# Optimization experiments

Measured on AMD Instinct MI355X. Metric: run time of the kernel, lower is better.

Reference implementation:

```python
import jax, jax.numpy as jnp
from jax import lax
import numpy as np

C_IN, C_OUT, K, STRIDE = 256, 512, 3, 1
EPS = 1e-5


def setup_inputs() -> dict:
    key = jax.random.key(0)
    ks = jax.random.split(key, 8)
    B, H, W = 32, 56, 56
    x = jax.random.normal(ks[0], (B, C_IN, H, W), dtype=jnp.float32)
    dw_w = jax.random.normal(ks[1], (C_IN, 1, K, K), dtype=jnp.float32) * 0.1
    dw_b = jax.random.normal(ks[2], (C_IN,), dtype=jnp.float32) * 0.05
    g1 = jnp.ones((C_IN,), dtype=jnp.float32)
    b1 = jnp.zeros((C_IN,), dtype=jnp.float32)
    pw_w = jax.random.normal(ks[3], (C_OUT, C_IN), dtype=jnp.float32) * (1.0 / np.sqrt(C_IN))
    pw_b = jax.random.normal(ks[4], (C_OUT,), dtype=jnp.float32) * 0.05
    g2 = jnp.ones((C_OUT,), dtype=jnp.float32)
    b2 = jnp.zeros((C_OUT,), dtype=jnp.float32)
    return {"x": x, "dw_w": dw_w, "dw_b": dw_b, "g1": g1, "b1": b1,
            "pw_w": pw_w, "pw_b": pw_b, "g2": g2, "b2": b2}


def _batchnorm(x, gamma, beta):
    # training-mode BN over (N, H, W) per channel, matching fresh nn.BatchNorm2d
    mean = jnp.mean(x, axis=(0, 2, 3), keepdims=True)
    var = jnp.var(x, axis=(0, 2, 3), keepdims=True)
    xn = (x - mean) * lax.rsqrt(var + EPS)
    return xn * gamma[None, :, None, None] + beta[None, :, None, None]


def reference(x, dw_w, dw_b, g1, b1, pw_w, pw_b, g2, b2):
    p = K // 2
    # reflect padding (padding_mode='reflect' in torch Conv2d)
    xp = jnp.pad(x, ((0, 0), (0, 0), (p, p), (p, p)), mode='reflect')
    # grouped depthwise conv: one filter per channel
    y = lax.conv_general_dilated(
        xp, dw_w, window_strides=(STRIDE, STRIDE), padding='VALID',
        dimension_numbers=('NCHW', 'OIHW', 'NCHW'),
        feature_group_count=C_IN)
    y = y + dw_b[None, :, None, None]
    y = jax.nn.relu(_batchnorm(y, g1, b1))
    # pointwise 1x1 conv == channel GEMM
    z = jnp.einsum('bchw,oc->bohw', y, pw_w) + pw_b[None, :, None, None]
    z = jax.nn.relu(_batchnorm(z, g2, b2))
    return z
```

## Files before the change

kernel.cpp:

```cpp
#include <hip/hip_runtime.h>
#include <hip/hip_bf16.h>
#include <stdint.h>


#define CIN   256
#define COUT  512
#define BATCH 32
#define HH    56
#define WWID  56
#define HWSZ  3136
#define NTOT  100352
#define NHWF  100352.0f
#define EPSV  1e-5f

typedef __bf16 bf16;
typedef __bf16 bf16x8 __attribute__((ext_vector_type(8)));
typedef float  f32x4  __attribute__((ext_vector_type(4)));

#define WS_STATS1   0
#define WS_SCALE1   2048
#define WS_SHIFT1   3072
#define WS_YSUM     4096
#define WS_S2       5120
#define WS_T2       7168
#define WS_G        16384
#define WS_WBF      278528
#define WS_YT       540672

__device__ __forceinline__ void gload16(const void* g, void* l) {
  __builtin_amdgcn_global_load_lds((const __attribute__((address_space(1))) void*)g,
                                   (__attribute__((address_space(3))) void*)l, 16, 0, 0);
}

__global__ __launch_bounds__(256) void k1_dwstats(const float* __restrict__ x,
                                                  const float* __restrict__ dww,
                                                  float* __restrict__ stats1) {
  __shared__ float plane[HWSZ];
  __shared__ float red[8];
  int bid = blockIdx.x;
  int c = bid & (CIN - 1);
  int b = bid >> 8;
  const float4* xp4 = (const float4*)(x + ((size_t)(b * CIN + c)) * HWSZ);
  float4* pl4 = (float4*)plane;
  for (int i = threadIdx.x; i < HWSZ / 4; i += 256) pl4[i] = xp4[i];
  float w9[9];
#pragma unroll
  for (int q = 0; q < 9; ++q) w9[q] = dww[c * 9 + q];
  __syncthreads();
  float s = 0.f, sq = 0.f;
  for (int p = threadIdx.x; p < HWSZ; p += 256) {
    int h = p / WWID;
    int w = p - h * WWID;
    float acc = 0.f;
#pragma unroll
    for (int dy = 0; dy < 3; ++dy) {
      int hh = h - 1 + dy;
      hh = hh < 0 ? 1 : (hh > 55 ? 54 : hh);
#pragma unroll
      for (int dx = 0; dx < 3; ++dx) {
        int ww2 = w - 1 + dx;
        ww2 = ww2 < 0 ? 1 : (ww2 > 55 ? 54 : ww2);
        acc += w9[dy * 3 + dx] * plane[hh * WWID + ww2];
      }
    }
    s += acc; sq += acc * acc;
  }
#pragma unroll
  for (int m = 1; m < 64; m <<= 1) { s += __shfl_xor(s, m); sq += __shfl_xor(sq, m); }
  int wv = threadIdx.x >> 6;
  if ((threadIdx.x & 63) == 0) { red[wv] = s; red[4 + wv] = sq; }
  __syncthreads();
  if (threadIdx.x == 0) {
    atomicAdd(&stats1[c],        red[0] + red[1] + red[2] + red[3]);
    atomicAdd(&stats1[CIN + c],  red[4] + red[5] + red[6] + red[7]);
  }
}

__global__ __launch_bounds__(256) void k2_finalize1(const float* __restrict__ stats1,
                                                    const float* __restrict__ g1,
                                                    const float* __restrict__ b1,
                                                    const float* __restrict__ pww,
                                                    float* __restrict__ scale1,
                                                    float* __restrict__ shift1,
                                                    bf16* __restrict__ wbf) {
  int blk = blockIdx.x, t = threadIdx.x;
  if (blk == 0) {
    float mean = stats1[t] * (1.0f / NHWF);
    float var  = stats1[CIN + t] * (1.0f / NHWF) - mean * mean;
    float sc = g1[t] * rsqrtf(var + EPSV);
    scale1[t] = sc;
    shift1[t] = b1[t] - mean * sc;
  } else {
    int o = blk - 1;
    wbf[o * CIN + t] = (bf16)pww[o * CIN + t];
  }
}

__global__ __launch_bounds__(256) void k3_normT(const float* __restrict__ x,
                                                const float* __restrict__ dww,
                                                const float* __restrict__ scale1,
                                                const float* __restrict__ shift1,
                                                bf16* __restrict__ yt) {
  __shared__ float xt[64][3][58];
  __shared__ __align__(16) bf16 outt[56][64];
  int bid = blockIdx.x;
  int cg = bid & 3;
  int h  = (bid >> 2) % 56;
  int b  = bid / 224;
  int c0 = cg * 64;
  int hr0 = (h == 0) ? 1 : h - 1;
  int hr2 = (h == 55) ? 54 : h + 1;
  for (int idx = threadIdx.x; idx < 64 * 3 * 56; idx += 256) {
    int c = idx / 168;
    int rem = idx - c * 168;
    int r = rem / 56;
    int w = rem - r * 56;
    int hr = (r == 0) ? hr0 : ((r == 1) ? h : hr2);
    xt[c][r][w + 1] = x[((size_t)((b * CIN + c0 + c) * HH + hr)) * WWID + w];
  }
  __syncthreads();
  if (threadIdx.x < 192) {
    int c = threadIdx.x / 3, r = threadIdx.x % 3;
    xt[c][r][0]  = xt[c][r][2];
    xt[c][r][57] = xt[c][r][55];
  }
  __syncthreads();
  int c  = threadIdx.x >> 2;
  int wq = threadIdx.x & 3;
  float w9[9];
#pragma unroll
  for (int q = 0; q < 9; ++q) w9[q] = dww[(c0 + c) * 9 + q];
  float sc = scale1[c0 + c], sh = shift1[c0 + c];
  for (int w = wq; w < 56; w += 4) {
    float acc = 0.f;
#pragma unroll
    for (int r = 0; r < 3; ++r) {
      const float* row = &xt[c][r][w];
      acc += w9[r * 3 + 0] * row[0] + w9[r * 3 + 1] * row[1] + w9[r * 3 + 2] * row[2];
    }
    float v = fmaxf(acc * sc + sh, 0.f);
    outt[w][c] = (bf16)v;
  }
  __syncthreads();
  for (int idx = threadIdx.x; idx < 56 * 8; idx += 256) {
    int w = idx >> 3, part = idx & 7;
    uint4 v = *(const uint4*)(&outt[w][part * 8]);
    *(uint4*)(yt + ((size_t)(b * HWSZ + h * WWID + w)) * CIN + c0 + part * 8) = v;
  }
}

__global__ __launch_bounds__(256) void kg_gram(const bf16* __restrict__ yt,
                                               float* __restrict__ G,
                                               float* __restrict__ ysum) {
  __shared__ __align__(16) unsigned short yTl[256 * 64];
  int bid = blockIdx.x;
  int job = bid & 3;
  int chunk = bid >> 2;
  int qa = job >> 1, qb = job & 1;
  int tid = threadIdx.x;
  int wv = tid >> 6, l = tid & 63;
  int wm = wv >> 1, wn = wv & 1;
  f32x4 acc[4][4];
#pragma unroll
  for (int mi = 0; mi < 4; ++mi)
#pragma unroll
    for (int ni = 0; ni < 4; ++ni) acc[mi][ni] = (f32x4){0.f, 0.f, 0.f, 0.f};
  float ys = 0.f;
  int r_loc = tid >> 2;
  int ci0 = tid & 3;
  int rs_k[8];
#pragma unroll
  for (int k = 0; k < 8; ++k) rs_k[k] = (r_loc & 7) | (((r_loc >> 3) ^ k) << 3);

  for (int it = 0; it < 16; ++it) {
    const unsigned short* src = (const unsigned short*)yt + ((size_t)chunk * 1024 + it * 64 + r_loc) * CIN;
#pragma unroll
    for (int u = 0; u < 8; ++u) {
      int c0 = (ci0 + u * 4) * 8;
      unsigned short v8[8];
      *(uint4*)v8 = *(const uint4*)(src + c0);
#pragma unroll
      for (int k = 0; k < 8; ++k) yTl[(c0 + k) * 64 + rs_k[k]] = v8[k];
    }
    __syncthreads();
#pragma unroll
    for (int kk = 0; kk < 2; ++kk) {
      bf16x8 af[4], bfr[4];
      int rc = kk * 4 + (l >> 4);
#pragma unroll
      for (int mi = 0; mi < 4; ++mi) {
        int c = qa * 128 + wm * 64 + mi * 16 + (l & 15);
        af[mi] = *(const bf16x8*)(yTl + c * 64 + ((rc ^ (c & 7)) << 3));
      }
#pragma unroll
      for (int ni = 0; ni < 4; ++ni) {
        int c = qb * 128 + wn * 64 + ni * 16 + (l & 15);
        bfr[ni] = *(const bf16x8*)(yTl + c * 64 + ((rc ^ (c & 7)) << 3));
      }
#pragma unroll
      for (int mi = 0; mi < 4; ++mi)
#pragma unroll
        for (int ni = 0; ni < 4; ++ni)
          acc[mi][ni] = __builtin_amdgcn_mfma_f32_16x16x32_bf16(af[mi], bfr[ni], acc[mi][ni], 0, 0, 0);
    }
    if (job == 0) {
      const bf16* row = (const bf16*)(yTl + tid * 64);
#pragma unroll
      for (int i = 0; i < 64; ++i) ys += (float)row[i];
    }
    __syncthreads();
  }
#pragma unroll
  for (int mi = 0; mi < 4; ++mi)
#pragma unroll
    for (int ni = 0; ni < 4; ++ni)
#pragma unroll
      for (int j = 0; j < 4; ++j) {
        int m = qa * 128 + wm * 64 + mi * 16 + (l >> 4) * 4 + j;
        int n = qb * 128 + wn * 64 + ni * 16 + (l & 15);
        atomicAdd(&G[m * 256 + n], acc[mi][ni][j]);
      }
  if (job == 0) atomicAdd(&ysum[tid], ys);
}

__global__ __launch_bounds__(256) void k2c_fin2(const float* __restrict__ G,
                                                const float* __restrict__ ysum,
                                                const bf16* __restrict__ wbf,
                                                const float* __restrict__ g2,
                                                const float* __restrict__ b2,
                                                float* __restrict__ s2,
                                                float* __restrict__ t2) {
  __shared__ float wl[256];
  __shared__ float red[8];
  int o = blockIdx.x, t = threadIdx.x;
  wl[t] = (float)wbf[o * 256 + t];
  __syncthreads();
  float gw = 0.f;
  for (int c = 0; c < 256; ++c) gw += G[c * 256 + t] * wl[c];
  float msq_p  = gw * wl[t];
  float mean_p = wl[t] * ysum[t];
#pragma unroll
  for (int m = 1; m < 64; m <<= 1) { msq_p += __shfl_xor(msq_p, m); mean_p += __shfl_xor(mean_p, m); }
  int wv = t >> 6;
  if ((t & 63) == 0) { red[wv] = msq_p; red[4 + wv] = mean_p; }
  __syncthreads();
  if (t == 0) {
    float msq  = (red[0] + red[1] + red[2] + red[3]) * (1.0f / NHWF);
    float mean = (red[4] + red[5] + red[6] + red[7]) * (1.0f / NHWF);
    float var  = msq - mean * mean;
    float sc = g2[o] * rsqrtf(var + EPSV);
    s2[o] = sc;
    t2[o] = b2[o] - mean * sc;
  }
}

__global__ __launch_bounds__(256) void k4_gemm(const bf16* __restrict__ wbf,
                                               const bf16* __restrict__ yt,
                                               const float* __restrict__ s2,
                                               const float* __restrict__ t2,
                                               float* __restrict__ out) {
  __shared__ __align__(16) unsigned char LDSBUF[32768];
  __shared__ float s2l[128], t2l[128];
  unsigned char* Als = LDSBUF;
  unsigned char* Bls = LDSBUF + 16384;
  int wg = blockIdx.x;
  int newid = (wg & 7) * 392 + (wg >> 3);
  int mt    = newid & 3;
  int ntile = newid >> 2;
  int tid = threadIdx.x;
  int wv = tid >> 6, l = tid & 63;
  int wm = wv >> 1, wn = wv & 1;
  if (tid < 128) { s2l[tid] = s2[mt * 128 + tid]; t2l[tid] = t2[mt * 128 + tid]; }
  f32x4 acc[4][4];
#pragma unroll
  for (int mi = 0; mi < 4; ++mi)
#pragma unroll
    for (int ni = 0; ni < 4; ++ni) acc[mi][ni] = (f32x4){0.f, 0.f, 0.f, 0.f};
  const char* wb = (const char*)wbf;
  const char* yb = (const char*)yt + (size_t)ntile * 128 * CIN * 2;

  for (int k0 = 0; k0 < 256; k0 += 64) {
#pragma unroll
    for (int i = 0; i < 4; ++i) {
      int q = i * 256 + wv * 64 + l;
      int row = q >> 3, pp = q & 7;
      int cc = pp ^ (row & 7);
      gload16(wb + ((size_t)(mt * 128 + row) * CIN + k0) * 2 + cc * 16,
              Als + i * 4096 + wv * 1024);
      gload16(yb + ((size_t)row * CIN + k0) * 2 + cc * 16,
              Bls + i * 4096 + wv * 1024);
    }
    __syncthreads();
#pragma unroll
    for (int kk = 0; kk < 2; ++kk) {
      bf16x8 af[4], bfr[4];
#pragma unroll
      for (int mi = 0; mi < 4; ++mi) {
        int row = wm * 64 + mi * 16 + (l & 15);
        int ck = kk * 4 + (l >> 4);
        af[mi] = *(const bf16x8*)(Als + row * 128 + ((ck ^ (row & 7)) << 4));
      }
#pragma unroll
      for (int ni = 0; ni < 4; ++ni) {
        int row = wn * 64 + ni * 16 + (l & 15);
        int ck = kk * 4 + (l >> 4);
        bfr[ni] = *(const bf16x8*)(Bls + row * 128 + ((ck ^ (row & 7)) << 4));
      }
#pragma unroll
      for (int mi = 0; mi < 4; ++mi)
#pragma unroll
        for (int ni = 0; ni < 4; ++ni)
          acc[mi][ni] = __builtin_amdgcn_mfma_f32_16x16x32_bf16(af[mi], bfr[ni], acc[mi][ni], 0, 0, 0);
    }
    __syncthreads();
  }

#pragma unroll
  for (int mi = 0; mi < 4; ++mi)
#pragma unroll
    for (int ni = 0; ni < 4; ++ni)
#pragma unroll
      for (int j = 0; j < 4; ++j) {
        int ol = wm * 64 + mi * 16 + (l >> 4) * 4 + j;
        int r_flat = ntile * 128 + wn * 64 + ni * 16 + (l & 15);
        int b  = r_flat / HWSZ;
        int hw = r_flat - b * HWSZ;
        float v = fmaxf(acc[mi][ni][j] * s2l[ol] + t2l[ol], 0.f);
        out[((size_t)(b * COUT + mt * 128 + ol)) * HWSZ + hw] = v;
      }
}

extern "C" void kernel_launch(void* const* d_in, const int* in_sizes, int n_in,
                              void* d_out, int out_size, void* d_ws, size_t ws_size,
                              hipStream_t stream) {
  const float* x   = (const float*)d_in[0];
  const float* dww = (const float*)d_in[1];
  const float* g1  = (const float*)d_in[3];
  const float* b1  = (const float*)d_in[4];
  const float* pww = (const float*)d_in[5];
  const float* g2  = (const float*)d_in[7];
  const float* b2  = (const float*)d_in[8];
  float* out = (float*)d_out;
  char* ws = (char*)d_ws;
  float* stats1 = (float*)(ws + WS_STATS1);
  float* scale1 = (float*)(ws + WS_SCALE1);
  float* shift1 = (float*)(ws + WS_SHIFT1);
  float* ysum   = (float*)(ws + WS_YSUM);
  float* s2     = (float*)(ws + WS_S2);
  float* t2     = (float*)(ws + WS_T2);
  float* G      = (float*)(ws + WS_G);
  bf16* wbf = (bf16*)(ws + WS_WBF);
  bf16* yt  = (bf16*)(ws + WS_YT);

  hipMemsetAsync(d_ws, 0, WS_WBF, stream);
  k1_dwstats<<<BATCH * CIN, 256, 0, stream>>>(x, dww, stats1);
  k2_finalize1<<<513, 256, 0, stream>>>(stats1, g1, b1, pww, scale1, shift1, wbf);
  k3_normT<<<BATCH * 56 * 4, 256, 0, stream>>>(x, dww, scale1, shift1, yt);
  kg_gram<<<392, 256, 0, stream>>>(yt, G, ysum);
  k2c_fin2<<<COUT, 256, 0, stream>>>(G, ysum, wbf, g2, b2, s2, t2);
  k4_gemm<<<3136, 256, 0, stream>>>(wbf, yt, s2, t2, out);
}
```

Baseline: 499.9 us.

## Store raw depthwise output in bf16 and rework transpose loads

The stats kernel now also writes the raw depthwise-conv result to a bf16 NCHW buffer. The normalize/transpose kernel reads that buffer instead of recomputing the 3x3 conv from fp32 x, which halves its read traffic and drops the conv math. The gram kernel's LDS transpose-fill is restructured to use wider 8-byte LDS stores. The cost is an extra 51 MB bf16 write and read of the intermediate, and normalization is now applied to a bf16-rounded pre-BN value, which adds a small precision loss.

```diff
diff --git a/kernel.cpp b/kernel.cpp
--- a/kernel.cpp
+++ b/kernel.cpp
@@ -26,15 +26,21 @@
 #define WS_G        16384
 #define WS_WBF      278528
 #define WS_YT       540672
+#define WS_YRAW     51920896
 
 __device__ __forceinline__ void gload16(const void* g, void* l) {
   __builtin_amdgcn_global_load_lds((const __attribute__((address_space(1))) void*)g,
                                    (__attribute__((address_space(3))) void*)l, 16, 0, 0);
 }
-
-__global__ __launch_bounds__(256) void k1_dwstats(const float* __restrict__ x,
-                                                  const float* __restrict__ dww,
-                                                  float* __restrict__ stats1) {
+__device__ __forceinline__ float bfu(unsigned int u16) {
+  unsigned int x = u16 << 16;
+  return __builtin_bit_cast(float, x);
+}
+
+__global__ __launch_bounds__(256) void k1_conv_stats(const float* __restrict__ x,
+                                                     const float* __restrict__ dww,
+                                                     float* __restrict__ stats1,
+                                                     bf16* __restrict__ yraw) {
   __shared__ float plane[HWSZ];
   __shared__ float red[8];
   int bid = blockIdx.x;
@@ -47,6 +53,7 @@
 #pragma unroll
   for (int q = 0; q < 9; ++q) w9[q] = dww[c * 9 + q];
   __syncthreads();
+  bf16* yout = yraw + ((size_t)(b * CIN + c)) * HWSZ;
   float s = 0.f, sq = 0.f;
   for (int p = threadIdx.x; p < HWSZ; p += 256) {
     int h = p / WWID;
@@ -64,6 +71,7 @@
       }
     }
     s += acc; sq += acc * acc;
+    yout[p] = (bf16)acc;
   }
 #pragma unroll
   for (int m = 1; m < 64; m <<= 1) { s += __shfl_xor(s, m); sq += __shfl_xor(sq, m); }
@@ -96,56 +104,42 @@
   }
 }
 
-__global__ __launch_bounds__(256) void k3_normT(const float* __restrict__ x,
-                                                const float* __restrict__ dww,
+__global__ __launch_bounds__(256) void k3_normT(const bf16* __restrict__ yraw,
                                                 const float* __restrict__ scale1,
                                                 const float* __restrict__ shift1,
                                                 bf16* __restrict__ yt) {
-  __shared__ float xt[64][3][58];
-  __shared__ __align__(16) bf16 outt[56][64];
+  __shared__ unsigned short tl[64 * 66];
   int bid = blockIdx.x;
-  int cg = bid & 3;
-  int h  = (bid >> 2) % 56;
-  int b  = bid / 224;
-  int c0 = cg * 64;
-  int hr0 = (h == 0) ? 1 : h - 1;
-  int hr2 = (h == 55) ? 54 : h + 1;
-  for (int idx = threadIdx.x; idx < 64 * 3 * 56; idx += 256) {
-    int c = idx / 168;
-    int rem = idx - c * 168;
-    int r = rem / 56;
-    int w = rem - r * 56;
-    int hr = (r == 0) ? hr0 : ((r == 1) ? h : hr2);
-    xt[c][r][w + 1] = x[((size_t)((b * CIN + c0 + c) * HH + hr)) * WWID + w];
-  }
-  __syncthreads();
-  if (threadIdx.x < 192) {
-    int c = threadIdx.x / 3, r = threadIdx.x % 3;
-    xt[c][r][0]  = xt[c][r][2];
-    xt[c][r][57] = xt[c][r][55];
-  }
-  __syncthreads();
-  int c  = threadIdx.x >> 2;
-  int wq = threadIdx.x & 3;
-  float w9[9];
-#pragma unroll
-  for (int q = 0; q < 9; ++q) w9[q] = dww[(c0 + c) * 9 + q];
-  float sc = scale1[c0 + c], sh = shift1[c0 + c];
-  for (int w = wq; w < 56; w += 4) {
-    float acc = 0.f;
-#pragma unroll
-    for (int r = 0; r < 3; ++r) {
-      const float* row = &xt[c][r][w];
-      acc += w9[r * 3 + 0] * row[0] + w9[r * 3 + 1] * row[1] + w9[r * 3 + 2] * row[2];
-    }
-    float v = fmaxf(acc * sc + sh, 0.f);
-    outt[w][c] = (bf16)v;
-  }
-  __syncthreads();
-  for (int idx = threadIdx.x; idx < 56 * 8; idx += 256) {
-    int w = idx >> 3, part = idx & 7;
-    uint4 v = *(const uint4*)(&outt[w][part * 8]);
-    *(uint4*)(yt + ((size_t)(b * HWSZ + h * WWID + w)) * CIN + c0 + part * 8) = v;
+  int hwt = bid % 49;
+  int cg  = (bid / 49) & 3;
+  int b   = bid / 196;
+  int t = threadIdx.x;
+  int cl = t >> 3, hq = t & 7;
+#pragma unroll
+  for (int hh = 0; hh < 2; ++hh) {
+    int c_l = cl + hh * 32;
+    int c = cg * 64 + c_l;
+    float sc = scale1[c], sh = shift1[c];
+    unsigned short v8[8];
+    *(uint4*)v8 = *(const uint4*)((const unsigned short*)yraw +
+                                  ((size_t)(b * CIN + c)) * HWSZ + hwt * 64 + hq * 8);
+#pragma unroll
+    for (int j = 0; j < 8; ++j) {
+      float v = fmaxf(bfu(v8[j]) * sc + sh, 0.f);
+      bf16 hb = (bf16)v;
+      tl[c_l * 66 + hq * 8 + j] = *(unsigned short*)&hb;
+    }
+  }
+  __syncthreads();
+  int rl = t >> 3, cq = t & 7;
+#pragma unroll
+  for (int hh = 0; hh < 2; ++hh) {
+    int r_l = rl + hh * 32;
+    unsigned short o8[8];
+#pragma unroll
+    for (int k = 0; k < 8; ++k) o8[k] = tl[(cq * 8 + k) * 66 + r_l];
+    *(uint4*)((unsigned short*)yt + ((size_t)(b * HWSZ + hwt * 64 + r_l)) * CIN + cg * 64 + cq * 8) =
+        *(uint4*)o8;
   }
 }
 
@@ -166,22 +160,27 @@
 #pragma unroll
     for (int ni = 0; ni < 4; ++ni) acc[mi][ni] = (f32x4){0.f, 0.f, 0.f, 0.f};
   float ys = 0.f;
-  int r_loc = tid >> 2;
-  int ci0 = tid & 3;
-  int rs_k[8];
-#pragma unroll
-  for (int k = 0; k < 8; ++k) rs_k[k] = (r_loc & 7) | (((r_loc >> 3) ^ k) << 3);
+  int rq  = tid & 15;
+  int cgp = tid >> 4;
 
   for (int it = 0; it < 16; ++it) {
-    const unsigned short* src = (const unsigned short*)yt + ((size_t)chunk * 1024 + it * 64 + r_loc) * CIN;
-#pragma unroll
-    for (int u = 0; u < 8; ++u) {
-      int c0 = (ci0 + u * 4) * 8;
-      unsigned short v8[8];
-      *(uint4*)v8 = *(const uint4*)(src + c0);
-#pragma unroll
-      for (int k = 0; k < 8; ++k) yTl[(c0 + k) * 64 + rs_k[k]] = v8[k];
-    }
+    const unsigned short* srcb = (const unsigned short*)yt +
+        ((size_t)chunk * 1024 + it * 64 + rq * 4) * CIN;
+    unsigned short v[2][4][8];
+#pragma unroll
+    for (int u = 0; u < 2; ++u)
+#pragma unroll
+      for (int j = 0; j < 4; ++j)
+        *(uint4*)v[u][j] = *(const uint4*)(srcb + (size_t)j * CIN + u * 128 + cgp * 8);
+#pragma unroll
+    for (int u = 0; u < 2; ++u)
+#pragma unroll
+      for (int k = 0; k < 8; ++k) {
+        int c = u * 128 + cgp * 8 + k;
+        int addr = c * 64 + (((rq >> 1) ^ k) << 3) + (rq & 1) * 4;
+        unsigned short o4[4] = {v[u][0][k], v[u][1][k], v[u][2][k], v[u][3][k]};
+        *(unsigned long long*)(yTl + addr) = *(const unsigned long long*)o4;
+      }
     __syncthreads();
 #pragma unroll
     for (int kk = 0; kk < 2; ++kk) {
@@ -349,13 +348,14 @@
   float* s2     = (float*)(ws + WS_S2);
   float* t2     = (float*)(ws + WS_T2);
   float* G      = (float*)(ws + WS_G);
-  bf16* wbf = (bf16*)(ws + WS_WBF);
-  bf16* yt  = (bf16*)(ws + WS_YT);
+  bf16* wbf  = (bf16*)(ws + WS_WBF);
+  bf16* yt   = (bf16*)(ws + WS_YT);
+  bf16* yraw = (bf16*)(ws + WS_YRAW);
 
   hipMemsetAsync(d_ws, 0, WS_WBF, stream);
-  k1_dwstats<<<BATCH * CIN, 256, 0, stream>>>(x, dww, stats1);
+  k1_conv_stats<<<BATCH * CIN, 256, 0, stream>>>(x, dww, stats1, yraw);
   k2_finalize1<<<513, 256, 0, stream>>>(stats1, g1, b1, pww, scale1, shift1, wbf);
-  k3_normT<<<BATCH * 56 * 4, 256, 0, stream>>>(x, dww, scale1, shift1, yt);
+  k3_normT<<<6272, 256, 0, stream>>>(yraw, scale1, shift1, yt);
   kg_gram<<<392, 256, 0, stream>>>(yt, G, ysum);
   k2c_fin2<<<COUT, 256, 0, stream>>>(G, ysum, wbf, g2, b2, s2, t2);
   k4_gemm<<<3136, 256, 0, stream>>>(wbf, yt, s2, t2, out);
```

Measured after the change: 408.6 us. 18.3% less time.
